# Kernel tuning notes

Hardware: AMD Instinct MI355X
Metric: run time of the kernel (lower is better)

Reference implementation:

```python
import jax, jax.numpy as jnp
import numpy as np

B, L, D, H, DK = 4, 256, 512, 8, 64
NEG_INF = 1.0e9


def setup_inputs() -> dict:
    key = jax.random.key(0)
    ks = jax.random.split(key, 12)
    s = 1.0 / np.sqrt(D)
    inp = {
        "q": jax.random.normal(ks[0], (B, L, D), jnp.float32),
        "k": jax.random.normal(ks[1], (B, L, D), jnp.float32),
        "v": jax.random.normal(ks[2], (B, L, D), jnp.float32),
        "mask": jnp.ones((B, L, L), jnp.int32),
        "Wq": jax.random.normal(ks[3], (D, D), jnp.float32) * s,
        "bq": jnp.zeros((D,), jnp.float32),
        "Wk": jax.random.normal(ks[4], (D, D), jnp.float32) * s,
        "bk": jnp.zeros((D,), jnp.float32),
        "Wv": jax.random.normal(ks[5], (D, D), jnp.float32) * s,
        "bv": jnp.zeros((D,), jnp.float32),
        "vp": jax.random.normal(ks[6], (1, H, 1, 1, DK), jnp.float32) * 0.1,
        "W0": jax.random.normal(ks[7], (D, D), jnp.float32) * s,
        "b0": jnp.zeros((D,), jnp.float32),
    }
    return inp


def reference(q, k, v, mask, Wq, bq, Wk, bk, Wv, bv, vp, W0, b0):
    # project and split heads: (B, L, D) -> (B, H, L, DK)
    qh = (q @ Wq + bq).reshape(B, L, H, DK).transpose(0, 2, 1, 3)
    kh = (k @ Wk + bk).reshape(B, L, H, DK).transpose(0, 2, 1, 3)
    vh = (v @ Wv + bv).reshape(B, L, H, DK).transpose(0, 2, 1, 3)
    # additive (Bahdanau) scoring: (B, H, Lq, Lk, DK) intermediate
    energy = jnp.tanh(qh[:, :, :, None, :] + kh[:, :, None, :, :])
    scores = jnp.sum(vp * energy, axis=-1)  # (B, H, Lq, Lk)
    scores = jnp.where(mask[:, None] == 0, -NEG_INF, scores)
    attn = jax.nn.softmax(scores, axis=-1)
    out = jnp.matmul(attn, vh)  # (B, H, Lq, DK)
    out = out.transpose(0, 2, 1, 3).reshape(B, L, D)
    return out @ W0 + b0
```

## Files before the change

kernel.cpp:

```cpp
#include <hip/hip_runtime.h>

#define LSEQ 256
#define DMODEL 512
#define NHEAD 8
#define DKH 64
#define BATCH 4

#define TWO_LOG2E 2.885390081777927f

using short8 = __attribute__((ext_vector_type(8))) short;
using f32x4  = __attribute__((ext_vector_type(4))) float;

__device__ __forceinline__ void split4(const float* f, ushort4& h, ushort4& l) {
  unsigned short hh[4], ll[4];
#pragma unroll
  for (int j = 0; j < 4; ++j) {
    unsigned int u = __float_as_uint(f[j]);
    hh[j] = (unsigned short)(u >> 16);
    float hf = __uint_as_float(u & 0xFFFF0000u);
    ll[j] = (unsigned short)(__float_as_uint(f[j] - hf) >> 16);
  }
  h = make_ushort4(hh[0], hh[1], hh[2], hh[3]);
  l = make_ushort4(ll[0], ll[1], ll[2], ll[3]);
}

__global__ __launch_bounds__(256) void prep_kernel(
    const float* __restrict__ q, const float* __restrict__ k, const float* __restrict__ v,
    const float* __restrict__ Wq, const float* __restrict__ Wk,
    const float* __restrict__ Wv, const float* __restrict__ W0,
    unsigned short* __restrict__ xhi, unsigned short* __restrict__ xlo,
    unsigned short* __restrict__ whi, unsigned short* __restrict__ wlo)
{
  const int z = blockIdx.z;
  const int tid = threadIdx.x;
  if (z < 3) {
    const float* X = (z == 0) ? q : (z == 1) ? k : v;
    const int r = blockIdx.x * 32 + (tid >> 3);
    const int c = blockIdx.y * 32 + ((tid & 7) << 2);
    float4 f = *(const float4*)&X[r * DMODEL + c];
    ushort4 h4, l4;
    split4((const float*)&f, h4, l4);
    const int base = (z * 1024 + r) * DMODEL + c;
    *(ushort4*)&xhi[base] = h4;
    *(ushort4*)&xlo[base] = l4;
  } else {
    if (blockIdx.x >= 16) return;
    const int g = z - 3;
    const float* W = (g == 0) ? Wq : (g == 1) ? Wk : (g == 2) ? Wv : W0;
    const float scale = (g < 2) ? TWO_LOG2E : 1.0f;
    const int k0 = blockIdx.x * 32, n0 = blockIdx.y * 32;
    __shared__ float tile[32][36];
    {
      const int r = tid >> 3, c = (tid & 7) << 2;
      float4 f = *(const float4*)&W[(k0 + r) * DMODEL + n0 + c];
      tile[r][c + 0] = f.x * scale;
      tile[r][c + 1] = f.y * scale;
      tile[r][c + 2] = f.z * scale;
      tile[r][c + 3] = f.w * scale;
    }
    __syncthreads();
    const int n = tid >> 3, kk = (tid & 7) << 2;
    float x[4];
#pragma unroll
    for (int j = 0; j < 4; ++j) x[j] = tile[kk + j][n];
    ushort4 h4, l4;
    split4(x, h4, l4);
    const int base = (g * DMODEL + n0 + n) * DMODEL + k0 + kk;
    *(ushort4*)&whi[base] = h4;
    *(ushort4*)&wlo[base] = l4;
  }
}

__device__ __forceinline__ void mfma_gemm(
    const unsigned short* __restrict__ xh, const unsigned short* __restrict__ xl,
    const unsigned short* __restrict__ wh, const unsigned short* __restrict__ wl,
    const float* __restrict__ bias, float bscale,
    float* __restrict__ out, int mode, int bx, int by)
{
  __shared__ short8 lds[2][4][256];
  const int tid = threadIdx.x;
  const int lane = tid & 63, w = tid >> 6;
  const int bm0 = bx * 64, bn0 = by * 64;

  const int r = tid >> 2, c = tid & 3;
  const int gch = (c ^ (r & 3)) << 3;
  const size_t aoff = (size_t)(bm0 + r) * DMODEL + gch;
  const size_t boff = (size_t)(bn0 + r) * DMODEL + gch;

  const int mrb = (w >> 1) << 5, ncb = (w & 1) << 5;
  const int l15 = lane & 15, lh = lane >> 4;

  const int ar0 = mrb + l15, ar1 = mrb + 16 + l15;
  const int as0 = ar0 * 4 + (lh ^ (ar0 & 3));
  const int as1 = ar1 * 4 + (lh ^ (ar1 & 3));
  const int br0 = ncb + l15, br1 = ncb + 16 + l15;
  const int bs0 = br0 * 4 + (lh ^ (br0 & 3));
  const int bs1 = br1 * 4 + (lh ^ (br1 & 3));

  short8 sah, sal, sbh, sbl;
#define LOADS(K)                                  \
  { sah = *(const short8*)(xh + aoff + (K));      \
    sal = *(const short8*)(xl + aoff + (K));      \
    sbh = *(const short8*)(wh + boff + (K));      \
    sbl = *(const short8*)(wl + boff + (K)); }
#define WRITES(BUF)                               \
  { lds[BUF][0][tid] = sah; lds[BUF][1][tid] = sal; \
    lds[BUF][2][tid] = sbh; lds[BUF][3][tid] = sbl; }

  f32x4 acc[2][2] = {};
  LOADS(0);
  WRITES(0);
  __syncthreads();

  for (int t = 0; t < 16; ++t) {
    if (t < 15) LOADS((t + 1) * 32);
    const int cur = t & 1;
    short8 a0h = lds[cur][0][as0], a0l = lds[cur][1][as0];
    short8 a1h = lds[cur][0][as1], a1l = lds[cur][1][as1];
    short8 b0h = lds[cur][2][bs0], b0l = lds[cur][3][bs0];
    short8 b1h = lds[cur][2][bs1], b1l = lds[cur][3][bs1];
#define MFMA_(A, B, C) C = __builtin_amdgcn_mfma_f32_16x16x32_bf16(A, B, C, 0, 0, 0)
    MFMA_(a0h, b0h, acc[0][0]); MFMA_(a0h, b0l, acc[0][0]); MFMA_(a0l, b0h, acc[0][0]);
    MFMA_(a0h, b1h, acc[0][1]); MFMA_(a0h, b1l, acc[0][1]); MFMA_(a0l, b1h, acc[0][1]);
    MFMA_(a1h, b0h, acc[1][0]); MFMA_(a1h, b0l, acc[1][0]); MFMA_(a1l, b0h, acc[1][0]);
    MFMA_(a1h, b1h, acc[1][1]); MFMA_(a1h, b1l, acc[1][1]); MFMA_(a1l, b1h, acc[1][1]);
#undef MFMA_
    if (t < 15) WRITES(cur ^ 1);
    __syncthreads();
  }
#undef LOADS
#undef WRITES

  const int bm = bm0 + mrb, bn = bn0 + ncb;
#pragma unroll
  for (int mi = 0; mi < 2; ++mi)
#pragma unroll
    for (int ni = 0; ni < 2; ++ni) {
      const int C = bn + ni * 16 + l15;
      const float bv = bscale * bias[C];
#pragma unroll
      for (int e = 0; e < 4; ++e) {
        const int R = bm + mi * 16 + (lh << 2) + e;
        const float val = acc[mi][ni][e] + bv;
        if (mode == 0) {
          out[R * DMODEL + C] = val;
        } else {
          const int b = R >> 8, l = R & (LSEQ - 1);
          const int hh = C >> 6, dk = C & 63;
          if (mode == 1) out[((b * NHEAD + hh) * LSEQ + l) * DKH + dk] = val;
          else           out[((b * NHEAD + hh) * DKH + dk) * LSEQ + l] = val;
        }
      }
    }
}

__global__ __launch_bounds__(256, 4) void proj_mfma_kernel(
    const unsigned short* __restrict__ xhi, const unsigned short* __restrict__ xlo,
    const unsigned short* __restrict__ whi, const unsigned short* __restrict__ wlo,
    const float* __restrict__ bq, const float* __restrict__ bk, const float* __restrict__ bv,
    float* __restrict__ qh, float* __restrict__ kT, float* __restrict__ vh)
{
  int lin = blockIdx.x + 16 * blockIdx.y + 128 * blockIdx.z;
  lin = (lin & 7) * 48 + (lin >> 3);
  const int bx = lin & 15, by = (lin >> 4) & 7, g = lin >> 7;
  const unsigned short* xh = xhi + (size_t)g * 1024 * DMODEL;
  const unsigned short* xl = xlo + (size_t)g * 1024 * DMODEL;
  const unsigned short* wh = whi + (size_t)g * DMODEL * DMODEL;
  const unsigned short* wl = wlo + (size_t)g * DMODEL * DMODEL;
  if (g == 0)      mfma_gemm(xh, xl, wh, wl, bq, TWO_LOG2E, qh, 1, bx, by);
  else if (g == 1) mfma_gemm(xh, xl, wh, wl, bk, TWO_LOG2E, kT, 2, bx, by);
  else             mfma_gemm(xh, xl, wh, wl, bv, 1.0f, vh, 1, bx, by);
}

__global__ __launch_bounds__(256, 4) void outproj_mfma_kernel(
    const unsigned short* __restrict__ aoh, const unsigned short* __restrict__ aol,
    const unsigned short* __restrict__ whi, const unsigned short* __restrict__ wlo,
    const float* __restrict__ b0, float* __restrict__ out)
{
  int lin = blockIdx.x + 16 * blockIdx.y;
  lin = (lin & 7) * 16 + (lin >> 3);
  const int bx = lin & 15, by = lin >> 4;
  mfma_gemm(aoh, aol, whi + (size_t)3 * DMODEL * DMODEL,
            wlo + (size_t)3 * DMODEL * DMODEL, b0, 1.0f, out, 0, bx, by);
}

__global__ __launch_bounds__(1024, 4) void attn_kernel(
    const float* __restrict__ qh,
    const float* __restrict__ kT,
    const float* __restrict__ vh,
    const int* __restrict__ mask,
    const float* __restrict__ vp,
    unsigned short* __restrict__ aoh,
    unsigned short* __restrict__ aol)
{
  __shared__ float ksh[DKH][LSEQ];
  __shared__ float vsh[LSEQ][DKH];
  __shared__ float qsh[32][DKH];
  __shared__ float psh[16][LSEQ];
  __shared__ float vpsh[DKH];

  const int bh = blockIdx.x;
  const int b = bh >> 3, h = bh & 7;
  const int i0 = blockIdx.y * 32;
  const int tid = threadIdx.x;
  const int lane = tid & 63, w = tid >> 6;

  const float* kbase = kT + (size_t)bh * DKH * LSEQ;
  for (int t = tid; t < DKH * LSEQ / 4; t += 1024) {
    const int d = t >> 6, j4 = (t & 63) << 2;
    *(float4*)&ksh[d][j4] = *(const float4*)&kbase[d * LSEQ + j4];
  }
  const float* vbase = vh + (size_t)bh * LSEQ * DKH;
  for (int t = tid; t < LSEQ * DKH / 4; t += 1024) {
    const int j = t >> 4, d4 = (t & 15) << 2;
    *(float4*)&vsh[j][d4] = *(const float4*)&vbase[j * DKH + d4];
  }
  if (tid < 512) {
    const float* qbase = qh + ((size_t)bh * LSEQ + i0) * DKH;
    const int r = tid >> 4, d4 = (tid & 15) << 2;
    *(float4*)&qsh[r][d4] = *(const float4*)&qbase[r * DKH + d4];
  }
  if (tid < DKH) vpsh[tid] = vp[h * DKH + tid];
  __syncthreads();

  float tj[2][4] = {};
#pragma unroll 2
  for (int g = 0; g < 16; ++g) {
    float kv[16];
#pragma unroll
    for (int t = 0; t < 4; ++t)
#pragma unroll
      for (int c = 0; c < 4; ++c)
        kv[t * 4 + c] = ksh[(g << 2) + t][(c << 6) + lane];
    float vpv[4];
    *(float4*)vpv = *(const float4*)&vpsh[g << 2];
#pragma unroll
    for (int r = 0; r < 2; ++r) {
      float q_[4];
      *(float4*)q_ = *(const float4*)&qsh[(w << 1) + r][g << 2];
#pragma unroll
      for (int t = 0; t < 4; ++t)
#pragma unroll
        for (int c = 0; c < 4; ++c) {
          const float x = q_[t] + kv[t * 4 + c];
          const float e = __builtin_amdgcn_exp2f(x);
          tj[r][c] = fmaf(vpv[t], __builtin_amdgcn_rcpf(e + 1.f), tj[r][c]);
        }
    }
  }

  const int cg = lane >> 4, qq = lane & 15;
#pragma unroll
  for (int r = 0; r < 2; ++r) {
    const int i = i0 + (w << 1) + r;
    const int* mrow = mask + ((size_t)b * LSEQ + i) * LSEQ;
    float t4[4];
#pragma unroll
    for (int c = 0; c < 4; ++c) {
      const int mv = mrow[(c << 6) + lane];
      t4[c] = mv ? tj[r][c] : 1.0e9f;
    }
    float m = fminf(fminf(t4[0], t4[1]), fminf(t4[2], t4[3]));
#pragma unroll
    for (int off = 32; off; off >>= 1) m = fminf(m, __shfl_xor(m, off));
    const float m2 = m * TWO_LOG2E;
    float p[4];
    float sum = 0.f;
#pragma unroll
    for (int c = 0; c < 4; ++c) {
      p[c] = __builtin_amdgcn_exp2f(fmaf(t4[c], -TWO_LOG2E, m2));
      sum += p[c];
    }
#pragma unroll
    for (int off = 32; off; off >>= 1) sum += __shfl_xor(sum, off);
    const float rs = __builtin_amdgcn_rcpf(sum);
#pragma unroll
    for (int c = 0; c < 4; ++c) psh[w][(c << 6) + lane] = p[c];

    float o[4] = {0.f, 0.f, 0.f, 0.f};
#pragma unroll 4
    for (int jg = 0; jg < 16; ++jg) {
      float pv[4];
      *(float4*)pv = *(const float4*)&psh[w][(cg << 6) + (jg << 2)];
#pragma unroll
      for (int t = 0; t < 4; ++t) {
        float v_[4];
        *(float4*)v_ = *(const float4*)&vsh[(cg << 6) + (jg << 2) + t][qq << 2];
#pragma unroll
        for (int u = 0; u < 4; ++u) o[u] = fmaf(pv[t], v_[u], o[u]);
      }
    }
#pragma unroll
    for (int off = 16; off <= 32; off <<= 1) {
#pragma unroll
      for (int u = 0; u < 4; ++u) o[u] += __shfl_xor(o[u], off);
    }
    if (lane < 16) {
      float ov[4];
#pragma unroll
      for (int u = 0; u < 4; ++u) ov[u] = o[u] * rs;
      ushort4 h4, l4;
      split4(ov, h4, l4);
      const int base = ((size_t)b * LSEQ + i) * DMODEL + h * DKH + (qq << 2);
      *(ushort4*)&aoh[base] = h4;
      *(ushort4*)&aol[base] = l4;
    }
  }
}

extern "C" void kernel_launch(void* const* d_in, const int* in_sizes, int n_in,
                              void* d_out, int out_size, void* d_ws, size_t ws_size,
                              hipStream_t stream) {
  const float* q   = (const float*)d_in[0];
  const float* k   = (const float*)d_in[1];
  const float* v   = (const float*)d_in[2];
  const int*  mask = (const int*)d_in[3];
  const float* Wq  = (const float*)d_in[4];
  const float* bq  = (const float*)d_in[5];
  const float* Wk  = (const float*)d_in[6];
  const float* bk  = (const float*)d_in[7];
  const float* Wv  = (const float*)d_in[8];
  const float* bv  = (const float*)d_in[9];
  const float* vp  = (const float*)d_in[10];
  const float* W0  = (const float*)d_in[11];
  const float* b0  = (const float*)d_in[12];
  float* outp = (float*)d_out;

  char* wsb = (char*)d_ws;
  unsigned short* whi = (unsigned short*)(wsb);
  unsigned short* wlo = (unsigned short*)(wsb + (2u << 20));
  unsigned short* xhi = (unsigned short*)(wsb + (4u << 20));
  unsigned short* xlo = (unsigned short*)(wsb + (7u << 20));
  float* qh = (float*)(wsb + (10u << 20));
  float* kT = (float*)(wsb + (12u << 20));
  float* vh = (float*)(wsb + (14u << 20));
  unsigned short* aoh = xhi;
  unsigned short* aol = xlo;

  prep_kernel<<<dim3(32, 16, 7), 256, 0, stream>>>(q, k, v, Wq, Wk, Wv, W0,
                                                   xhi, xlo, whi, wlo);
  proj_mfma_kernel<<<dim3(16, 8, 3), 256, 0, stream>>>(xhi, xlo, whi, wlo,
                                                       bq, bk, bv, qh, kT, vh);
  attn_kernel<<<dim3(32, 8), 1024, 0, stream>>>(qh, kT, vh, mask, vp, aoh, aol);
  outproj_mfma_kernel<<<dim3(16, 8), 256, 0, stream>>>(aoh, aol, whi, wlo, b0, outp);
}
```

Measured before the change: 143.8 us.

## Fuse all stages into one persistent kernel with software grid barriers

Replaces the four separate launches (prep, QKV projection, attention, output projection) with a single 256-block mega-kernel that separates phases with an atomic grid barrier, plus a tiny init kernel that resets the barrier counters. The GEMM phases drop the LDS double-buffered 64x64 tile and use per-wave 32x32 tiles that read directly from global memory, with only some waves active. The goal is to remove launch gaps and tail effects between stages. The trade-offs are GEMM phases with fewer active waves and no LDS reuse, barrier spin overhead, and reliance on all 256 blocks being co-resident. The LDS footprint of about 152 KB per block may limit occupancy to one block per CU.

```diff
diff --git a/kernel.cpp b/kernel.cpp
--- a/kernel.cpp
+++ b/kernel.cpp
@@ -5,6 +5,7 @@
 #define NHEAD 8
 #define DKH 64
 #define BATCH 4
+#define NBLK 256
 
 #define TWO_LOG2E 2.885390081777927f
 
@@ -24,114 +25,66 @@
   l = make_ushort4(ll[0], ll[1], ll[2], ll[3]);
 }
 
-__global__ __launch_bounds__(256) void prep_kernel(
-    const float* __restrict__ q, const float* __restrict__ k, const float* __restrict__ v,
-    const float* __restrict__ Wq, const float* __restrict__ Wk,
-    const float* __restrict__ Wv, const float* __restrict__ W0,
-    unsigned short* __restrict__ xhi, unsigned short* __restrict__ xlo,
-    unsigned short* __restrict__ whi, unsigned short* __restrict__ wlo)
-{
-  const int z = blockIdx.z;
-  const int tid = threadIdx.x;
-  if (z < 3) {
-    const float* X = (z == 0) ? q : (z == 1) ? k : v;
-    const int r = blockIdx.x * 32 + (tid >> 3);
-    const int c = blockIdx.y * 32 + ((tid & 7) << 2);
-    float4 f = *(const float4*)&X[r * DMODEL + c];
-    ushort4 h4, l4;
-    split4((const float*)&f, h4, l4);
-    const int base = (z * 1024 + r) * DMODEL + c;
-    *(ushort4*)&xhi[base] = h4;
-    *(ushort4*)&xlo[base] = l4;
-  } else {
-    if (blockIdx.x >= 16) return;
-    const int g = z - 3;
-    const float* W = (g == 0) ? Wq : (g == 1) ? Wk : (g == 2) ? Wv : W0;
-    const float scale = (g < 2) ? TWO_LOG2E : 1.0f;
-    const int k0 = blockIdx.x * 32, n0 = blockIdx.y * 32;
-    __shared__ float tile[32][36];
-    {
-      const int r = tid >> 3, c = (tid & 7) << 2;
-      float4 f = *(const float4*)&W[(k0 + r) * DMODEL + n0 + c];
-      tile[r][c + 0] = f.x * scale;
-      tile[r][c + 1] = f.y * scale;
-      tile[r][c + 2] = f.z * scale;
-      tile[r][c + 3] = f.w * scale;
-    }
-    __syncthreads();
-    const int n = tid >> 3, kk = (tid & 7) << 2;
-    float x[4];
-#pragma unroll
-    for (int j = 0; j < 4; ++j) x[j] = tile[kk + j][n];
-    ushort4 h4, l4;
-    split4(x, h4, l4);
-    const int base = (g * DMODEL + n0 + n) * DMODEL + k0 + kk;
-    *(ushort4*)&whi[base] = h4;
-    *(ushort4*)&wlo[base] = l4;
-  }
-}
-
-__device__ __forceinline__ void mfma_gemm(
+__device__ __forceinline__ void split8(float4 f0, float4 f1, short8& h, short8& l) {
+  float f[8] = {f0.x, f0.y, f0.z, f0.w, f1.x, f1.y, f1.z, f1.w};
+#pragma unroll
+  for (int j = 0; j < 8; ++j) {
+    unsigned int u = __float_as_uint(f[j]);
+    h[j] = (short)(u >> 16);
+    float hf = __uint_as_float(u & 0xFFFF0000u);
+    l[j] = (short)(__float_as_uint(f[j] - hf) >> 16);
+  }
+}
+
+__global__ void init_kernel(unsigned* bar) { bar[0] = 0u; bar[1] = 0u; }
+
+__device__ __forceinline__ void gbar(unsigned* cnt, unsigned* rel, unsigned phase) {
+  __syncthreads();
+  if (threadIdx.x == 0) {
+    __threadfence();
+    unsigned old = __hip_atomic_fetch_add(cnt, 1u, __ATOMIC_ACQ_REL,
+                                          __HIP_MEMORY_SCOPE_AGENT);
+    if (old == NBLK - 1) {
+      __hip_atomic_store(cnt, 0u, __ATOMIC_RELAXED, __HIP_MEMORY_SCOPE_AGENT);
+      __hip_atomic_store(rel, phase, __ATOMIC_RELEASE, __HIP_MEMORY_SCOPE_AGENT);
+    } else {
+      while (__hip_atomic_load(rel, __ATOMIC_ACQUIRE,
+                               __HIP_MEMORY_SCOPE_AGENT) < phase)
+        __builtin_amdgcn_s_sleep(2);
+      __threadfence();
+    }
+  }
+  __syncthreads();
+}
+
+__device__ __forceinline__ void gemm_tile32(
     const unsigned short* __restrict__ xh, const unsigned short* __restrict__ xl,
     const unsigned short* __restrict__ wh, const unsigned short* __restrict__ wl,
     const float* __restrict__ bias, float bscale,
-    float* __restrict__ out, int mode, int bx, int by)
+    float* __restrict__ out, int mode, int bm, int bn, int lane)
 {
-  __shared__ short8 lds[2][4][256];
-  const int tid = threadIdx.x;
-  const int lane = tid & 63, w = tid >> 6;
-  const int bm0 = bx * 64, bn0 = by * 64;
-
-  const int r = tid >> 2, c = tid & 3;
-  const int gch = (c ^ (r & 3)) << 3;
-  const size_t aoff = (size_t)(bm0 + r) * DMODEL + gch;
-  const size_t boff = (size_t)(bn0 + r) * DMODEL + gch;
-
-  const int mrb = (w >> 1) << 5, ncb = (w & 1) << 5;
   const int l15 = lane & 15, lh = lane >> 4;
-
-  const int ar0 = mrb + l15, ar1 = mrb + 16 + l15;
-  const int as0 = ar0 * 4 + (lh ^ (ar0 & 3));
-  const int as1 = ar1 * 4 + (lh ^ (ar1 & 3));
-  const int br0 = ncb + l15, br1 = ncb + 16 + l15;
-  const int bs0 = br0 * 4 + (lh ^ (br0 & 3));
-  const int bs1 = br1 * 4 + (lh ^ (br1 & 3));
-
-  short8 sah, sal, sbh, sbl;
-#define LOADS(K)                                  \
-  { sah = *(const short8*)(xh + aoff + (K));      \
-    sal = *(const short8*)(xl + aoff + (K));      \
-    sbh = *(const short8*)(wh + boff + (K));      \
-    sbl = *(const short8*)(wl + boff + (K)); }
-#define WRITES(BUF)                               \
-  { lds[BUF][0][tid] = sah; lds[BUF][1][tid] = sal; \
-    lds[BUF][2][tid] = sbh; lds[BUF][3][tid] = sbl; }
-
+  const int rA0 = bm + l15, rA1 = rA0 + 16;
+  const int cB0 = bn + l15, cB1 = cB0 + 16;
+  const int kb = lh << 3;
   f32x4 acc[2][2] = {};
-  LOADS(0);
-  WRITES(0);
-  __syncthreads();
-
-  for (int t = 0; t < 16; ++t) {
-    if (t < 15) LOADS((t + 1) * 32);
-    const int cur = t & 1;
-    short8 a0h = lds[cur][0][as0], a0l = lds[cur][1][as0];
-    short8 a1h = lds[cur][0][as1], a1l = lds[cur][1][as1];
-    short8 b0h = lds[cur][2][bs0], b0l = lds[cur][3][bs0];
-    short8 b1h = lds[cur][2][bs1], b1l = lds[cur][3][bs1];
+  for (int k0 = 0; k0 < DMODEL; k0 += 32) {
+    const int ko = k0 + kb;
+    short8 a0h = *(const short8*)(xh + (size_t)rA0 * DMODEL + ko);
+    short8 a0l = *(const short8*)(xl + (size_t)rA0 * DMODEL + ko);
+    short8 a1h = *(const short8*)(xh + (size_t)rA1 * DMODEL + ko);
+    short8 a1l = *(const short8*)(xl + (size_t)rA1 * DMODEL + ko);
+    short8 b0h = *(const short8*)(wh + (size_t)cB0 * DMODEL + ko);
+    short8 b0l = *(const short8*)(wl + (size_t)cB0 * DMODEL + ko);
+    short8 b1h = *(const short8*)(wh + (size_t)cB1 * DMODEL + ko);
+    short8 b1l = *(const short8*)(wl + (size_t)cB1 * DMODEL + ko);
 #define MFMA_(A, B, C) C = __builtin_amdgcn_mfma_f32_16x16x32_bf16(A, B, C, 0, 0, 0)
     MFMA_(a0h, b0h, acc[0][0]); MFMA_(a0h, b0l, acc[0][0]); MFMA_(a0l, b0h, acc[0][0]);
     MFMA_(a0h, b1h, acc[0][1]); MFMA_(a0h, b1l, acc[0][1]); MFMA_(a0l, b1h, acc[0][1]);
     MFMA_(a1h, b0h, acc[1][0]); MFMA_(a1h, b0l, acc[1][0]); MFMA_(a1l, b0h, acc[1][0]);
     MFMA_(a1h, b1h, acc[1][1]); MFMA_(a1h, b1l, acc[1][1]); MFMA_(a1l, b1h, acc[1][1]);
 #undef MFMA_
-    if (t < 15) WRITES(cur ^ 1);
-    __syncthreads();
-  }
-#undef LOADS
-#undef WRITES
-
-  const int bm = bm0 + mrb, bn = bn0 + ncb;
+  }
 #pragma unroll
   for (int mi = 0; mi < 2; ++mi)
 #pragma unroll
@@ -154,157 +107,211 @@
     }
 }
 
-__global__ __launch_bounds__(256, 4) void proj_mfma_kernel(
-    const unsigned short* __restrict__ xhi, const unsigned short* __restrict__ xlo,
-    const unsigned short* __restrict__ whi, const unsigned short* __restrict__ wlo,
-    const float* __restrict__ bq, const float* __restrict__ bk, const float* __restrict__ bv,
-    float* __restrict__ qh, float* __restrict__ kT, float* __restrict__ vh)
+__global__ __launch_bounds__(1024, 4) void mega_kernel(
+    const float* __restrict__ q, const float* __restrict__ k, const float* __restrict__ v,
+    const int* __restrict__ mask,
+    const float* __restrict__ Wq, const float* __restrict__ bq,
+    const float* __restrict__ Wk, const float* __restrict__ bk,
+    const float* __restrict__ Wv, const float* __restrict__ bv,
+    const float* __restrict__ vp,
+    const float* __restrict__ W0, const float* __restrict__ b0,
+    unsigned short* __restrict__ xhi, unsigned short* __restrict__ xlo,
+    unsigned short* __restrict__ whi, unsigned short* __restrict__ wlo,
+    float* __restrict__ qh, float* __restrict__ kT, float* __restrict__ vh,
+    unsigned short* __restrict__ aoh, unsigned short* __restrict__ aol,
+    unsigned* __restrict__ bar,
+    float* __restrict__ outp)
 {
-  int lin = blockIdx.x + 16 * blockIdx.y + 128 * blockIdx.z;
-  lin = (lin & 7) * 48 + (lin >> 3);
-  const int bx = lin & 15, by = (lin >> 4) & 7, g = lin >> 7;
-  const unsigned short* xh = xhi + (size_t)g * 1024 * DMODEL;
-  const unsigned short* xl = xlo + (size_t)g * 1024 * DMODEL;
-  const unsigned short* wh = whi + (size_t)g * DMODEL * DMODEL;
-  const unsigned short* wl = wlo + (size_t)g * DMODEL * DMODEL;
-  if (g == 0)      mfma_gemm(xh, xl, wh, wl, bq, TWO_LOG2E, qh, 1, bx, by);
-  else if (g == 1) mfma_gemm(xh, xl, wh, wl, bk, TWO_LOG2E, kT, 2, bx, by);
-  else             mfma_gemm(xh, xl, wh, wl, bv, 1.0f, vh, 1, bx, by);
-}
-
-__global__ __launch_bounds__(256, 4) void outproj_mfma_kernel(
-    const unsigned short* __restrict__ aoh, const unsigned short* __restrict__ aol,
-    const unsigned short* __restrict__ whi, const unsigned short* __restrict__ wlo,
-    const float* __restrict__ b0, float* __restrict__ out)
-{
-  int lin = blockIdx.x + 16 * blockIdx.y;
-  lin = (lin & 7) * 16 + (lin >> 3);
-  const int bx = lin & 15, by = lin >> 4;
-  mfma_gemm(aoh, aol, whi + (size_t)3 * DMODEL * DMODEL,
-            wlo + (size_t)3 * DMODEL * DMODEL, b0, 1.0f, out, 0, bx, by);
-}
-
-__global__ __launch_bounds__(1024, 4) void attn_kernel(
-    const float* __restrict__ qh,
-    const float* __restrict__ kT,
-    const float* __restrict__ vh,
-    const int* __restrict__ mask,
-    const float* __restrict__ vp,
-    unsigned short* __restrict__ aoh,
-    unsigned short* __restrict__ aol)
-{
-  __shared__ float ksh[DKH][LSEQ];
-  __shared__ float vsh[LSEQ][DKH];
-  __shared__ float qsh[32][DKH];
-  __shared__ float psh[16][LSEQ];
-  __shared__ float vpsh[DKH];
-
-  const int bh = blockIdx.x;
-  const int b = bh >> 3, h = bh & 7;
-  const int i0 = blockIdx.y * 32;
+  __shared__ __align__(16) char smem[155904];
+  float (*ksh)[LSEQ] = (float(*)[LSEQ])(smem);
+  float (*vsh)[DKH]  = (float(*)[DKH])(smem + 65536);
+  float (*qsh)[DKH]  = (float(*)[DKH])(smem + 131072);
+  float (*psh)[LSEQ] = (float(*)[LSEQ])(smem + 139264);
+  float* vpsh        = (float*)(smem + 155648);
+
+  const int bx = blockIdx.x;
   const int tid = threadIdx.x;
-  const int lane = tid & 63, w = tid >> 6;
-
-  const float* kbase = kT + (size_t)bh * DKH * LSEQ;
-  for (int t = tid; t < DKH * LSEQ / 4; t += 1024) {
-    const int d = t >> 6, j4 = (t & 63) << 2;
-    *(float4*)&ksh[d][j4] = *(const float4*)&kbase[d * LSEQ + j4];
-  }
-  const float* vbase = vh + (size_t)bh * LSEQ * DKH;
-  for (int t = tid; t < LSEQ * DKH / 4; t += 1024) {
-    const int j = t >> 4, d4 = (t & 15) << 2;
-    *(float4*)&vsh[j][d4] = *(const float4*)&vbase[j * DKH + d4];
-  }
-  if (tid < 512) {
-    const float* qbase = qh + ((size_t)bh * LSEQ + i0) * DKH;
-    const int r = tid >> 4, d4 = (tid & 15) << 2;
-    *(float4*)&qsh[r][d4] = *(const float4*)&qbase[r * DKH + d4];
-  }
-  if (tid < DKH) vpsh[tid] = vp[h * DKH + tid];
-  __syncthreads();
-
-  float tj[2][4] = {};
+  const int lane = tid & 63, wv = tid >> 6;
+  unsigned* cnt = bar;
+  unsigned* rel = bar + 1;
+
+  {
+    float (*tile)[32][36] = (float(*)[32][36])smem;
+    const int tsub = tid >> 8;
+    const int sub = tid & 255;
+    const int tile_id = bx * 4 + tsub;
+    const int g = tile_id >> 8;
+    const int rem = tile_id & 255;
+    const int k0 = (rem & 15) * 32, n0 = (rem >> 4) * 32;
+    const float* W = (g == 0) ? Wq : (g == 1) ? Wk : (g == 2) ? Wv : W0;
+    const float scale = (g < 2) ? TWO_LOG2E : 1.0f;
+    {
+      const int r = sub >> 3, c = (sub & 7) << 2;
+      float4 f = *(const float4*)&W[(k0 + r) * DMODEL + n0 + c];
+      tile[tsub][r][c + 0] = f.x * scale;
+      tile[tsub][r][c + 1] = f.y * scale;
+      tile[tsub][r][c + 2] = f.z * scale;
+      tile[tsub][r][c + 3] = f.w * scale;
+    }
+    __syncthreads();
+    {
+      const int n = sub >> 3, kk = (sub & 7) << 2;
+      float x[4];
+#pragma unroll
+      for (int j = 0; j < 4; ++j) x[j] = tile[tsub][kk + j][n];
+      ushort4 h4, l4;
+      split4(x, h4, l4);
+      const int base = (g * DMODEL + n0 + n) * DMODEL + k0 + kk;
+      *(ushort4*)&whi[base] = h4;
+      *(ushort4*)&wlo[base] = l4;
+    }
+    const int idx = bx * 1024 + tid;
+    if (idx < 196608) {
+      const int e = idx * 8;
+      const int z = e >> 19;
+      const int off = e & 524287;
+      const float* Xs = (z == 0) ? q : (z == 1) ? k : v;
+      float4 f0 = *(const float4*)(Xs + off);
+      float4 f1 = *(const float4*)(Xs + off + 4);
+      short8 h_, l_;
+      split8(f0, f1, h_, l_);
+      *(short8*)(xhi + (size_t)z * 524288 + off) = h_;
+      *(short8*)(xlo + (size_t)z * 524288 + off) = l_;
+    }
+  }
+  gbar(cnt, rel, 1u);
+
+  if (wv < 6) {
+    const int t = bx * 6 + wv;
+    const int g = t >> 9;
+    const int r512 = t & 511;
+    const int bm = (r512 & 31) << 5, bn = (r512 >> 5) << 5;
+    const unsigned short* xh = xhi + (size_t)g * 524288;
+    const unsigned short* xl = xlo + (size_t)g * 524288;
+    const unsigned short* wh = whi + (size_t)g * 262144;
+    const unsigned short* wl = wlo + (size_t)g * 262144;
+    const float* bias = (g == 0) ? bq : (g == 1) ? bk : bv;
+    const float bscale = (g < 2) ? TWO_LOG2E : 1.0f;
+    float* out = (g == 0) ? qh : (g == 1) ? kT : vh;
+    const int mode = (g == 1) ? 2 : 1;
+    gemm_tile32(xh, xl, wh, wl, bias, bscale, out, mode, bm, bn, lane);
+  }
+  gbar(cnt, rel, 2u);
+
+  {
+    const int bh = bx >> 3;
+    const int b = bh >> 3, h = bh & 7;
+    const int i0 = (bx & 7) << 5;
+
+    const float* kbase = kT + (size_t)bh * DKH * LSEQ;
+    for (int t = tid; t < DKH * LSEQ / 4; t += 1024) {
+      const int d = t >> 6, j4 = (t & 63) << 2;
+      *(float4*)&ksh[d][j4] = *(const float4*)&kbase[d * LSEQ + j4];
+    }
+    const float* vbase = vh + (size_t)bh * LSEQ * DKH;
+    for (int t = tid; t < LSEQ * DKH / 4; t += 1024) {
+      const int j = t >> 4, d4 = (t & 15) << 2;
+      *(float4*)&vsh[j][d4] = *(const float4*)&vbase[j * DKH + d4];
+    }
+    if (tid < 512) {
+      const float* qbase = qh + ((size_t)bh * LSEQ + i0) * DKH;
+      const int r = tid >> 4, d4 = (tid & 15) << 2;
+      *(float4*)&qsh[r][d4] = *(const float4*)&qbase[r * DKH + d4];
+    }
+    if (tid < DKH) vpsh[tid] = vp[h * DKH + tid];
+    __syncthreads();
+
+    float tj[2][4] = {};
 #pragma unroll 2
-  for (int g = 0; g < 16; ++g) {
-    float kv[16];
-#pragma unroll
-    for (int t = 0; t < 4; ++t)
-#pragma unroll
-      for (int c = 0; c < 4; ++c)
-        kv[t * 4 + c] = ksh[(g << 2) + t][(c << 6) + lane];
-    float vpv[4];
-    *(float4*)vpv = *(const float4*)&vpsh[g << 2];
+    for (int g = 0; g < 16; ++g) {
+      float kv[16];
+#pragma unroll
+      for (int t = 0; t < 4; ++t)
+#pragma unroll
+        for (int c = 0; c < 4; ++c)
+          kv[t * 4 + c] = ksh[(g << 2) + t][(c << 6) + lane];
+      float vpv[4];
+      *(float4*)vpv = *(const float4*)&vpsh[g << 2];
+#pragma unroll
+      for (int r = 0; r < 2; ++r) {
+        float q_[4];
+        *(float4*)q_ = *(const float4*)&qsh[(wv << 1) + r][g << 2];
+#pragma unroll
+        for (int t = 0; t < 4; ++t)
+#pragma unroll
+          for (int c = 0; c < 4; ++c) {
+            const float x = q_[t] + kv[t * 4 + c];
+            const float e = __builtin_amdgcn_exp2f(x);
+            tj[r][c] = fmaf(vpv[t], __builtin_amdgcn_rcpf(e + 1.f), tj[r][c]);
+          }
+      }
+    }
+
+    const int cg = lane >> 4, qq = lane & 15;
 #pragma unroll
     for (int r = 0; r < 2; ++r) {
-      float q_[4];
-      *(float4*)q_ = *(const float4*)&qsh[(w << 1) + r][g << 2];
-#pragma unroll
-      for (int t = 0; t < 4; ++t)
-#pragma unroll
-        for (int c = 0; c < 4; ++c) {
-          const float x = q_[t] + kv[t * 4 + c];
-          const float e = __builtin_amdgcn_exp2f(x);
-          tj[r][c] = fmaf(vpv[t], __builtin_amdgcn_rcpf(e + 1.f), tj[r][c]);
+      const int i = i0 + (wv << 1) + r;
+      const int* mrow = mask + ((size_t)b * LSEQ + i) * LSEQ;
+      float t4[4];
+#pragma unroll
+      for (int c = 0; c < 4; ++c) {
+        const int mv = mrow[(c << 6) + lane];
+        t4[c] = mv ? tj[r][c] : 1.0e9f;
+      }
+      float m = fminf(fminf(t4[0], t4[1]), fminf(t4[2], t4[3]));
+#pragma unroll
+      for (int off = 32; off; off >>= 1) m = fminf(m, __shfl_xor(m, off));
+      const float m2 = m * TWO_LOG2E;
+      float p[4];
+      float sum = 0.f;
+#pragma unroll
+      for (int c = 0; c < 4; ++c) {
+        p[c] = __builtin_amdgcn_exp2f(fmaf(t4[c], -TWO_LOG2E, m2));
+        sum += p[c];
+      }
+#pragma unroll
+      for (int off = 32; off; off >>= 1) sum += __shfl_xor(sum, off);
+      const float rs = __builtin_amdgcn_rcpf(sum);
+#pragma unroll
+      for (int c = 0; c < 4; ++c) psh[wv][(c << 6) + lane] = p[c];
+
+      float o[4] = {0.f, 0.f, 0.f, 0.f};
+#pragma unroll 4
+      for (int jg = 0; jg < 16; ++jg) {
+        float pv[4];
+        *(float4*)pv = *(const float4*)&psh[wv][(cg << 6) + (jg << 2)];
+#pragma unroll
+        for (int t = 0; t < 4; ++t) {
+          float v_[4];
+          *(float4*)v_ = *(const float4*)&vsh[(cg << 6) + (jg << 2) + t][qq << 2];
+#pragma unroll
+          for (int u = 0; u < 4; ++u) o[u] = fmaf(pv[t], v_[u], o[u]);
         }
-    }
-  }
-
-  const int cg = lane >> 4, qq = lane & 15;
-#pragma unroll
-  for (int r = 0; r < 2; ++r) {
-    const int i = i0 + (w << 1) + r;
-    const int* mrow = mask + ((size_t)b * LSEQ + i) * LSEQ;
-    float t4[4];
-#pragma unroll
-    for (int c = 0; c < 4; ++c) {
-      const int mv = mrow[(c << 6) + lane];
-      t4[c] = mv ? tj[r][c] : 1.0e9f;
-    }
-    float m = fminf(fminf(t4[0], t4[1]), fminf(t4[2], t4[3]));
-#pragma unroll
-    for (int off = 32; off; off >>= 1) m = fminf(m, __shfl_xor(m, off));
-    const float m2 = m * TWO_LOG2E;
-    float p[4];
-    float sum = 0.f;
-#pragma unroll
-    for (int c = 0; c < 4; ++c) {
-      p[c] = __builtin_amdgcn_exp2f(fmaf(t4[c], -TWO_LOG2E, m2));
-      sum += p[c];
-    }
-#pragma unroll
-    for (int off = 32; off; off >>= 1) sum += __shfl_xor(sum, off);
-    const float rs = __builtin_amdgcn_rcpf(sum);
-#pragma unroll
-    for (int c = 0; c < 4; ++c) psh[w][(c << 6) + lane] = p[c];
-
-    float o[4] = {0.f, 0.f, 0.f, 0.f};
-#pragma unroll 4
-    for (int jg = 0; jg < 16; ++jg) {
-      float pv[4];
-      *(float4*)pv = *(const float4*)&psh[w][(cg << 6) + (jg << 2)];
-#pragma unroll
-      for (int t = 0; t < 4; ++t) {
-        float v_[4];
-        *(float4*)v_ = *(const float4*)&vsh[(cg << 6) + (jg << 2) + t][qq << 2];
-#pragma unroll
-        for (int u = 0; u < 4; ++u) o[u] = fmaf(pv[t], v_[u], o[u]);
-      }
-    }
-#pragma unroll
-    for (int off = 16; off <= 32; off <<= 1) {
-#pragma unroll
-      for (int u = 0; u < 4; ++u) o[u] += __shfl_xor(o[u], off);
-    }
-    if (lane < 16) {
-      float ov[4];
-#pragma unroll
-      for (int u = 0; u < 4; ++u) ov[u] = o[u] * rs;
-      ushort4 h4, l4;
-      split4(ov, h4, l4);
-      const int base = ((size_t)b * LSEQ + i) * DMODEL + h * DKH + (qq << 2);
-      *(ushort4*)&aoh[base] = h4;
-      *(ushort4*)&aol[base] = l4;
-    }
+      }
+#pragma unroll
+      for (int off = 16; off <= 32; off <<= 1) {
+#pragma unroll
+        for (int u = 0; u < 4; ++u) o[u] += __shfl_xor(o[u], off);
+      }
+      if (lane < 16) {
+        float ov[4];
+#pragma unroll
+        for (int u = 0; u < 4; ++u) ov[u] = o[u] * rs;
+        ushort4 h4, l4;
+        split4(ov, h4, l4);
+        const int base = ((size_t)b * LSEQ + i) * DMODEL + h * DKH + (qq << 2);
+        *(ushort4*)&aoh[base] = h4;
+        *(ushort4*)&aol[base] = l4;
+      }
+    }
+  }
+  gbar(cnt, rel, 3u);
+
+  if (wv == 0 || wv == 2) {
+    const int t = bx * 2 + (wv >> 1);
+    const int bm = (t & 31) << 5, bn = (t >> 5) << 5;
+    gemm_tile32(aoh, aol, whi + (size_t)3 * 262144, wlo + (size_t)3 * 262144,
+                b0, 1.0f, outp, 0, bm, bn, lane);
   }
 }
 
@@ -334,13 +341,12 @@
   float* qh = (float*)(wsb + (10u << 20));
   float* kT = (float*)(wsb + (12u << 20));
   float* vh = (float*)(wsb + (14u << 20));
-  unsigned short* aoh = xhi;
-  unsigned short* aol = xlo;
-
-  prep_kernel<<<dim3(32, 16, 7), 256, 0, stream>>>(q, k, v, Wq, Wk, Wv, W0,
-                                                   xhi, xlo, whi, wlo);
-  proj_mfma_kernel<<<dim3(16, 8, 3), 256, 0, stream>>>(xhi, xlo, whi, wlo,
-                                                       bq, bk, bv, qh, kT, vh);
-  attn_kernel<<<dim3(32, 8), 1024, 0, stream>>>(qh, kT, vh, mask, vp, aoh, aol);
-  outproj_mfma_kernel<<<dim3(16, 8), 256, 0, stream>>>(aoh, aol, whi, wlo, b0, outp);
-}
+  unsigned short* aoh = (unsigned short*)(wsb + (16u << 20));
+  unsigned short* aol = (unsigned short*)(wsb + (17u << 20));
+  unsigned* bar = (unsigned*)(wsb + (18u << 20));
+
+  init_kernel<<<1, 1, 0, stream>>>(bar);
+  mega_kernel<<<NBLK, 1024, 0, stream>>>(q, k, v, mask, Wq, bq, Wk, bk, Wv, bv,
+                                         vp, W0, b0, xhi, xlo, whi, wlo,
+                                         qh, kT, vh, aoh, aol, bar, outp);
+}
```

After: 266.9 us. 1.86x slower.
